# Kernel optimization log

Hardware: AMD Instinct MI355X
Metric: run time of the kernel (lower is better)

Reference implementation:

```python
import jax, jax.numpy as jnp
import numpy as np

NP, NC, E, EL = 50000, 5000, 200000, 100000
DP, DC, HID, OUT, HEADS = 1280, 256, 128, 128, 4


def setup_inputs() -> dict:
    key = jax.random.key(0)
    ks = jax.random.split(key, 40)
    p = lambda k, shp: jax.random.normal(k, shp, dtype=jnp.float32) * 0.05
    inp = {
        "x_protein": jax.random.normal(ks[0], (NP, DP), dtype=jnp.float32),
        "x_class": jax.random.normal(ks[1], (NC, DC), dtype=jnp.float32),
        "src": jax.random.randint(ks[2], (E,), 0, NP),
        "dst": jax.random.randint(ks[3], (E,), 0, NC),
        "edge_label_src": jax.random.randint(ks[4], (EL,), 0, NP),
        "edge_label_dst": jax.random.randint(ks[5], (EL,), 0, NC),
        # SAGEConv, relation protein->class (updates class nodes)
        "sage_pc_Wl": p(ks[6], (DP, HID)), "sage_pc_bl": p(ks[7], (HID,)), "sage_pc_Wr": p(ks[8], (DC, HID)),
        # SAGEConv, relation class->protein (updates protein nodes)
        "sage_cp_Wl": p(ks[9], (DC, HID)), "sage_cp_bl": p(ks[10], (HID,)), "sage_cp_Wr": p(ks[11], (DP, HID)),
        # GATConv p->c (inputs are hidden after conv1)
        "gat_pc_Wsrc": p(ks[12], (HID, HEADS * HID)), "gat_pc_Wdst": p(ks[13], (HID, HEADS * HID)),
        "gat_pc_asrc": p(ks[14], (HEADS, HID)), "gat_pc_adst": p(ks[15], (HEADS, HID)), "gat_pc_b": p(ks[16], (HID,)),
        # GATConv c->p
        "gat_cp_Wsrc": p(ks[17], (HID, HEADS * HID)), "gat_cp_Wdst": p(ks[18], (HID, HEADS * HID)),
        "gat_cp_asrc": p(ks[19], (HEADS, HID)), "gat_cp_adst": p(ks[20], (HEADS, HID)), "gat_cp_b": p(ks[21], (HID,)),
        # final per-node-type Linear (to_hetero duplicates lin per node type)
        "lin_p_W": p(ks[22], (HID, OUT)), "lin_p_b": p(ks[23], (OUT,)),
        "lin_c_W": p(ks[24], (HID, OUT)), "lin_c_b": p(ks[25], (OUT,)),
        # link predictor
        "link_W": p(ks[26], (2 * OUT, 1)), "link_b": p(ks[27], (1,)),
    }
    return inp


def _sage(x_src, x_dst, s, d, Wl, bl, Wr, n_dst):
    # PyG SAGEConv: lin_l(mean_aggr(x_src)) + lin_r(x_dst); lin_l has bias.
    agg = jax.ops.segment_sum(x_src[s], d, num_segments=n_dst)
    cnt = jax.ops.segment_sum(jnp.ones((s.shape[0], 1), x_src.dtype), d, num_segments=n_dst)
    mean = agg / jnp.maximum(cnt, 1.0)
    return mean @ Wl + bl + x_dst @ Wr


def _gat(x_src, x_dst, s, d, Ws, Wd, a_s, a_d, b, n_dst):
    # PyG GATConv bipartite, heads=HEADS, concat=False, add_self_loops=False.
    H, C = a_s.shape
    hs = (x_src @ Ws).reshape(-1, H, C)   # [Ns, H, C]
    hd = (x_dst @ Wd).reshape(-1, H, C)   # [Nd, H, C]
    als = jnp.einsum('nhc,hc->nh', hs, a_s)
    ald = jnp.einsum('nhc,hc->nh', hd, a_d)
    e = jax.nn.leaky_relu(als[s] + ald[d], 0.2)                    # [E, H]
    emax = jax.ops.segment_max(e, d, num_segments=n_dst)          # stable softmax per dst
    ee = jnp.exp(e - emax[d])
    denom = jax.ops.segment_sum(ee, d, num_segments=n_dst)
    alpha = ee / denom[d]                                          # [E, H]
    out = jax.ops.segment_sum(alpha[:, :, None] * hs[s], d, num_segments=n_dst)  # [Nd, H, C]
    return out.mean(axis=1) + b  # concat=False -> mean over heads


def reference(x_protein, x_class, src, dst, edge_label_src, edge_label_dst,
              sage_pc_Wl, sage_pc_bl, sage_pc_Wr,
              sage_cp_Wl, sage_cp_bl, sage_cp_Wr,
              gat_pc_Wsrc, gat_pc_Wdst, gat_pc_asrc, gat_pc_adst, gat_pc_b,
              gat_cp_Wsrc, gat_cp_Wdst, gat_cp_asrc, gat_cp_adst, gat_cp_b,
              lin_p_W, lin_p_b, lin_c_W, lin_c_b, link_W, link_b):
    # Layer 1: hetero SAGE (each node type has exactly one incoming relation)
    h_c = jax.nn.relu(_sage(x_protein, x_class, src, dst, sage_pc_Wl, sage_pc_bl, sage_pc_Wr, NC))
    h_p = jax.nn.relu(_sage(x_class, x_protein, dst, src, sage_cp_Wl, sage_cp_bl, sage_cp_Wr, NP))
    # Layer 2: hetero GAT
    g_c = jax.nn.relu(_gat(h_p, h_c, src, dst, gat_pc_Wsrc, gat_pc_Wdst, gat_pc_asrc, gat_pc_adst, gat_pc_b, NC))
    g_p = jax.nn.relu(_gat(h_c, h_p, dst, src, gat_cp_Wsrc, gat_cp_Wdst, gat_cp_asrc, gat_cp_adst, gat_cp_b, NP))
    # Per-type output projection
    z_p = g_p @ lin_p_W + lin_p_b
    z_c = g_c @ lin_c_W + lin_c_b
    # Link predictor: gather, concat, linear, sigmoid
    ef = jnp.concatenate([z_p[edge_label_src], z_c[edge_label_dst]], axis=-1)  # [EL, 2*OUT]
    return jax.nn.sigmoid(ef @ link_W + link_b).squeeze(-1)
```

## Files before the change

### kernel.cpp

```cpp
#include <hip/hip_runtime.h>
#include <math.h>

#define NPROT 50000
#define NCLS  5000
#define DIMP  1280
#define DIMC  256
#define SCAN_N (NCLS + NPROT)
#define KSTEPS (DIMP/32)

#define P1B  ((NPROT+127)/128)
#define C1BY ((NCLS+63)/64)
#define C1B  (4*C1BY)

typedef float4 f4;
typedef __attribute__((ext_vector_type(8))) short short8;
typedef __attribute__((ext_vector_type(4))) float f32x4;

__device__ __forceinline__ unsigned short f2bf(float f){
    unsigned u = __float_as_uint(f);
    u += 0x7FFFu + ((u >> 16) & 1u);
    return (unsigned short)(u >> 16);
}
__device__ __forceinline__ float bf2f(unsigned short b){
    return __uint_as_float(((unsigned)b) << 16);
}
__device__ __forceinline__ void gload_lds16(const void* g, void* l){
    __builtin_amdgcn_global_load_lds((const __attribute__((address_space(1))) void*)g,
                                     (__attribute__((address_space(3))) void*)l, 16, 0, 0);
}
__device__ __forceinline__ int OFFV(const int* __restrict__ offv, const int* __restrict__ part, int v){
    return offv[v] + part[v>>10];
}

__global__ __launch_bounds__(512) void mega1(const float* __restrict__ Af,
                                             const unsigned short* __restrict__ BtP,
                                             unsigned short* __restrict__ P1,
                                             const float* __restrict__ Ac,
                                             const float* __restrict__ WcatC,
                                             float* __restrict__ C1,
                                             const int* __restrict__ src, const int* __restrict__ dst,
                                             const int* __restrict__ offv, const int* __restrict__ part,
                                             int* __restrict__ cur, int* __restrict__ adj, int E){
    __shared__ __align__(16) unsigned char smem[64*1024];
    const int blk = blockIdx.x;
    const int tid = threadIdx.x;

    if(blk < P1B){
        unsigned char* As = smem;
        unsigned char* Bs = smem + 32*1024;
        const int lane = tid & 63;
        const int w    = tid >> 6;
        const int wm   = w >> 2, wn = w & 3;
        const int row0 = blk * 128;
        const int kg = lane >> 4, fr = lane & 15;

        f32x4 acc[4][4] = {};

        auto STAGE = [&](int buf, int k0){
            unsigned char* Ab = As + buf*16384;
            unsigned char* Bb = Bs + buf*16384;
            #pragma unroll
            for(int i=0;i<2;i++){
                int c  = i*512 + tid;
                int r  = c >> 3, cc = c & 7;
                int scc = cc ^ (r & 7);
                int srow = min(row0 + r, NPROT-1);
                gload_lds16((const void*)(Af + (size_t)srow*DIMP + k0 + scc*4),
                            (void*)(Ab + (i*512 + w*64 + lane)*16));
            }
            #pragma unroll
            for(int i=0;i<2;i++){
                int c  = i*512 + tid;
                int r  = c >> 2, cc = c & 3;
                int scc = cc ^ ((r>>1) & 3);
                gload_lds16((const void*)(BtP + (size_t)r*DIMP + k0 + scc*8),
                            (void*)(Bb + (i*512 + w*64 + lane)*16));
            }
        };

        STAGE(0, 0);
        __syncthreads();

        for(int t=0; t<KSTEPS; ++t){
            const int cb = t & 1;
            if(t+1 < KSTEPS) STAGE(cb^1, (t+1)*32);
            const unsigned char* Ab = As + cb*16384;
            const unsigned char* Bb = Bs + cb*16384;

            short8 aF[4], bF[4];
            #pragma unroll
            for(int m=0;m<4;m++){
                int r = wm*64 + m*16 + fr;
                int b0 = r*128 + kg*32;
                f4 lo = *(const f4*)(Ab + (( b0      ) ^ ((r&7)<<4)));
                f4 hi = *(const f4*)(Ab + (( b0 + 16 ) ^ ((r&7)<<4)));
                union { short8 s; unsigned short u[8]; } uu;
                uu.u[0]=f2bf(lo.x); uu.u[1]=f2bf(lo.y); uu.u[2]=f2bf(lo.z); uu.u[3]=f2bf(lo.w);
                uu.u[4]=f2bf(hi.x); uu.u[5]=f2bf(hi.y); uu.u[6]=f2bf(hi.z); uu.u[7]=f2bf(hi.w);
                aF[m] = uu.s;
            }
            #pragma unroll
            for(int n=0;n<4;n++){
                int r = wn*64 + n*16 + fr;
                int b0 = (r*64 + kg*16) ^ (((r>>1)&3)<<4);
                bF[n] = *(const short8*)(Bb + b0);
            }
            #pragma unroll
            for(int m=0;m<4;m++)
            #pragma unroll
            for(int n=0;n<4;n++)
                acc[m][n] = __builtin_amdgcn_mfma_f32_16x16x32_bf16(aF[m], bF[n], acc[m][n], 0, 0, 0);
            __syncthreads();
        }

        #pragma unroll
        for(int m=0;m<4;m++)
        #pragma unroll
        for(int r=0;r<4;r++){
            int row = row0 + wm*64 + m*16 + kg*4 + r;
            if(row < NPROT){
                #pragma unroll
                for(int n=0;n<4;n++)
                    P1[(size_t)row*256 + wn*64 + n*16 + fr] = f2bf(acc[m][n][r]);
            }
        }
    } else if(blk < P1B + C1B){
        float (*As)[68] = (float(*)[68])smem;
        float (*Bs)[64] = (float(*)[64])(smem + 16*68*4);
        const int bi = blk - P1B;
        const int row0 = (bi >> 2) * 64;
        const int col0 = (bi & 3) * 64;
        const bool act = tid < 256;
        const int ty = tid >> 4;
        const int tx = tid & 15;
        const int m  = tid >> 2;
        const int kq = (tid & 3) << 2;
        const int kb = tid >> 4;
        const int c4 = (tid & 15) << 2;

        float acc[4][4];
        #pragma unroll
        for(int i=0;i<4;i++)
        #pragma unroll
            for(int j=0;j<4;j++) acc[i][j]=0.f;

        const bool arow_ok = act && (row0 + m) < NCLS;
        const float* Abase = Ac + (size_t)(row0 + min(m,255)) * DIMC + kq;
        const float* Bbase = WcatC + col0 + c4 + (size_t)kb * 256;

        for(int k0 = 0; k0 < DIMC; k0 += 16){
            if(act){
                f4 av;
                if(arow_ok) av = *(const f4*)(Abase + k0);
                else        av = make_float4(0.f,0.f,0.f,0.f);
                As[kq+0][m]=av.x; As[kq+1][m]=av.y; As[kq+2][m]=av.z; As[kq+3][m]=av.w;
                *(f4*)&Bs[kb][c4] = *(const f4*)(Bbase + (size_t)k0 * 256);
            }
            __syncthreads();
            if(act){
                #pragma unroll
                for(int kk=0;kk<16;kk++){
                    f4 a = *(const f4*)&As[kk][ty<<2];
                    f4 b = *(const f4*)&Bs[kk][tx<<2];
                    float ar[4]={a.x,a.y,a.z,a.w};
                    float br[4]={b.x,b.y,b.z,b.w};
                    #pragma unroll
                    for(int i=0;i<4;i++)
                    #pragma unroll
                        for(int j=0;j<4;j++) acc[i][j] += ar[i]*br[j];
                }
            }
            __syncthreads();
        }
        if(act){
            #pragma unroll
            for(int i=0;i<4;i++){
                int r = row0 + (ty<<2) + i;
                if(r < NCLS){
                    f4 v = make_float4(acc[i][0],acc[i][1],acc[i][2],acc[i][3]);
                    *(f4*)&C1[(size_t)r*256 + col0 + (tx<<2)] = v;
                }
            }
        }
    } else {
        int e = (blk - P1B - C1B)*512 + tid;
        if(e < E){
            int s = src[e], d = dst[e];
            int pc = atomicAdd(&cur[d],1);        adj[OFFV(offv,part,d)+pc] = s;
            int pp = atomicAdd(&cur[NCLS+s],1);   adj[OFFV(offv,part,NCLS+s)+pp] = d;
        }
    }
}

#define NPB ((NPROT+127)/128)
#define NCB ((NCLS+127)/128)
__global__ __launch_bounds__(256) void gemm_hs(const unsigned short* __restrict__ Ap,
                                               const unsigned short* __restrict__ Ac,
                                               const unsigned short* __restrict__ Btp,
                                               const unsigned short* __restrict__ Btc,
                                               const float* __restrict__ projP,
                                               const float* __restrict__ projC,
                                               unsigned short* __restrict__ Cp,
                                               unsigned short* __restrict__ Cc,
                                               float* __restrict__ attP,
                                               float* __restrict__ attC){
    const bool cls = (int)blockIdx.y >= NPB;
    const unsigned short* A  = cls ? Ac : Ap;
    const unsigned short* Bt = cls ? Btc : Btp;
    unsigned short* C = cls ? Cc : Cp;
    const int M = cls ? NCLS : NPROT;
    const int row0 = (cls ? blockIdx.y - NPB : blockIdx.y) * 128;
    const int col0 = blockIdx.x * 128;

    __shared__ __align__(16) unsigned char As[128*32*2];
    __shared__ __align__(16) unsigned char Bs[128*32*2];
    __shared__ float projS[1024];
    const int tid  = threadIdx.x;
    const int lane = tid & 63;
    const int w    = tid >> 6;
    const int wm   = w >> 1, wn = w & 1;
    const int kg = lane >> 4, fr = lane & 15;

    f32x4 acc[4][4] = {};

    for(int k0 = 0; k0 < 128; k0 += 32){
        #pragma unroll
        for(int i=0;i<2;i++){
            int c  = i*256 + w*64 + lane;
            int r  = c >> 2, cc = c & 3;
            int scc = cc ^ ((r>>1) & 3);
            int srow = min(row0 + r, M-1);
            gload_lds16((const void*)(A + (size_t)srow*128 + k0 + scc*8),
                        (void*)(As + (i*256 + w*64)*16));
        }
        #pragma unroll
        for(int i=0;i<2;i++){
            int c  = i*256 + w*64 + lane;
            int r  = c >> 2, cc = c & 3;
            int scc = cc ^ ((r>>1) & 3);
            gload_lds16((const void*)(Bt + (size_t)(col0 + r)*128 + k0 + scc*8),
                        (void*)(Bs + (i*256 + w*64)*16));
        }
        __syncthreads();

        short8 aF[4], bF[4];
        #pragma unroll
        for(int m=0;m<4;m++){
            int r = wm*64 + m*16 + fr;
            int b0 = (r*64 + kg*16) ^ (((r>>1)&3)<<4);
            aF[m] = *(const short8*)(As + b0);
        }
        #pragma unroll
        for(int n=0;n<4;n++){
            int r = wn*64 + n*16 + fr;
            int b0 = (r*64 + kg*16) ^ (((r>>1)&3)<<4);
            bF[n] = *(const short8*)(Bs + b0);
        }
        #pragma unroll
        for(int m=0;m<4;m++)
        #pragma unroll
        for(int n=0;n<4;n++)
            acc[m][n] = __builtin_amdgcn_mfma_f32_16x16x32_bf16(aF[m], bF[n], acc[m][n], 0, 0, 0);
        __syncthreads();
    }

    #pragma unroll
    for(int m=0;m<4;m++)
    #pragma unroll
    for(int r=0;r<4;r++){
        int row = row0 + wm*64 + m*16 + kg*4 + r;
        if(row < M){
            #pragma unroll
            for(int n=0;n<4;n++)
                C[(size_t)row*512 + col0 + wn*64 + n*16 + fr] = f2bf(acc[m][n][r]);
        }
    }

    if(blockIdx.x == 0){
        const float* proj = cls ? projC : projP;
        float* att = cls ? attC : attP;
        for(int i=tid;i<1024;i+=256) projS[i] = proj[i];
        __syncthreads();
        int ri = tid >> 1, cb = (tid & 1)*4;
        int row = row0 + ri;
        if(row < M){
            const unsigned short* ar = A + (size_t)row*128;
            float s0=0.f,s1=0.f,s2=0.f,s3=0.f;
            #pragma unroll
            for(int kk=0;kk<16;kk++){
                short8 a8 = *(const short8*)(ar + kk*8);
                #pragma unroll
                for(int q=0;q<8;q++){
                    float av = bf2f((unsigned short)a8[q]);
                    const float* pr = &projS[(kk*8+q)*8 + cb];
                    s0 += av*pr[0]; s1 += av*pr[1]; s2 += av*pr[2]; s3 += av*pr[3];
                }
            }
            f4 o = make_float4(s0,s1,s2,s3);
            *(f4*)&att[(size_t)row*8 + cb] = o;
        }
    }
}

__global__ void setup(const float* __restrict__ Wl_pc, const float* __restrict__ Wr_cp,
                      const float* __restrict__ Wl_cp, const float* __restrict__ Wr_pc,
                      const float* __restrict__ pcWs, const float* __restrict__ pcAs,
                      const float* __restrict__ pcWd, const float* __restrict__ pcAd,
                      const float* __restrict__ cpWs, const float* __restrict__ cpAs,
                      const float* __restrict__ cpWd, const float* __restrict__ cpAd,
                      const float* __restrict__ lpW, const float* __restrict__ lpb,
                      const float* __restrict__ lcW, const float* __restrict__ lcb,
                      const float* __restrict__ linkW,
                      const int* __restrict__ src, const int* __restrict__ dst,
                      unsigned short* __restrict__ BtP, float* __restrict__ WcatC,
                      unsigned short* __restrict__ BtSp, unsigned short* __restrict__ BtSc,
                      float* __restrict__ projP, float* __restrict__ projC,
                      float* __restrict__ w_p, float* __restrict__ w_c,
                      float* __restrict__ cpc,
                      int* __restrict__ deg, int E){
    int blk = blockIdx.x, tid = threadIdx.x;
    if(blk < 2048){
        int t = blk*256 + tid;
        if(t < 327680){
            int n = t / 1280, k = t % 1280;
            float v = (n<128) ? Wl_pc[(size_t)k*128+n] : Wr_cp[(size_t)k*128+n-128];
            BtP[t] = f2bf(v);
        } else if(t < 393216){
            int i = t - 327680; int k = i>>8, j = i&255;
            WcatC[i] = (j<128) ? Wl_cp[(size_t)k*128+j] : Wr_pc[(size_t)k*128+j-128];
        } else if(t < 458752){
            int i = t - 393216; int n = i>>7, k = i&127;
            BtSp[i] = f2bf(pcWs[(size_t)k*512+n]);
        } else {
            int i = t - 458752; int n = i>>7, k = i&127;
            BtSc[i] = f2bf(cpWs[(size_t)k*512+n]);
        }
    } else if(blk < 2056){
        int sec = (blk-2048) >> 1;
        int t = ((blk-2048) & 1)*256 + tid;
        const float *W, *a; float* proj; int colbase;
        if(sec==0){ W=pcWs; a=pcAs; proj=projP; colbase=0; }
        else if(sec==1){ W=cpWd; a=cpAd; proj=projP; colbase=4; }
        else if(sec==2){ W=pcWd; a=pcAd; proj=projC; colbase=0; }
        else { W=cpWs; a=cpAs; proj=projC; colbase=4; }
        int k = t >> 2, h = t & 3;
        const float* w = W + (size_t)k*512 + h*128;
        const float* av = a + h*128;
        float s=0.f;
        for(int c=0;c<128;c++) s += w[c]*av[c];
        proj[k*8 + colbase + h] = s;
    } else if(blk == 2056){
        if(tid < 128){
            float s=0.f;
            for(int o=0;o<128;o++) s += lpW[(size_t)tid*128+o]*linkW[o];
            w_p[tid]=s;
        } else {
            int j=tid-128;
            float s=0.f;
            for(int o=0;o<128;o++) s += lcW[(size_t)j*128+o]*linkW[128+o];
            w_c[j]=s;
        }
        if(tid==0){ float s=0.f; for(int o=0;o<128;o++) s+=lpb[o]*linkW[o];      cpc[0]=s; }
        if(tid==1){ float s=0.f; for(int o=0;o<128;o++) s+=lcb[o]*linkW[128+o];  cpc[1]=s; }
    } else {
        int e = (blk-2057)*256 + tid;
        if(e < E){
            atomicAdd(&deg[dst[e]],1);
            atomicAdd(&deg[NCLS + src[e]],1);
        }
    }
}

__global__ __launch_bounds__(1024) void scan1(const int* __restrict__ in, int* __restrict__ out,
                                              int* __restrict__ part, int n){
    __shared__ int buf[1024];
    int tid = threadIdx.x;
    int g = blockIdx.x*1024 + tid;
    int v = (g<n) ? in[g] : 0;
    buf[tid] = v;
    __syncthreads();
    for(int o=1;o<1024;o<<=1){
        int t = (tid>=o) ? buf[tid-o] : 0;
        __syncthreads();
        buf[tid] += t;
        __syncthreads();
    }
    if(g<n) out[g] = buf[tid] - v;
    if(tid==1023) part[blockIdx.x] = buf[1023];
}
__global__ __launch_bounds__(64) void scan2(int* __restrict__ part, int nb,
                                            int* __restrict__ offv, int n){
    int tid = threadIdx.x;
    int orig = (tid<nb) ? part[tid] : 0;
    int v = orig;
    #pragma unroll
    for(int o=1;o<64;o<<=1){
        int t = __shfl_up(v, o);
        if(tid>=o) v += t;
    }
    int total = __shfl(v, nb-1);
    if(tid<nb) part[tid] = v - orig;
    if(tid == (n>>10)) offv[n] = total - (v - orig);
}

__global__ __launch_bounds__(256) void sage_all(const int* __restrict__ offv, const int* __restrict__ part,
                                                const int* __restrict__ adj,
                                                const unsigned short* __restrict__ P1, const float* __restrict__ C1,
                                                const float* __restrict__ bl_pc, const float* __restrict__ bl_cp,
                                                unsigned short* __restrict__ h_c, unsigned short* __restrict__ h_p){
    int v = blockIdx.x*4 + (threadIdx.x>>6);
    int l = threadIdx.x & 63;
    if(v >= SCAN_N) return;
    int b = OFFV(offv,part,v), deg = OFFV(offv,part,v+1)-b;
    float a0=0.f, a1=0.f;
    float inv = 1.f/(float)max(deg,1);
    if(v < NCLS){
        for(int i=0;i<deg;i++){
            int s = adj[b+i];
            ushort2 w = *((const ushort2*)P1 + (size_t)s*128 + l);
            a0 += bf2f(w.x); a1 += bf2f(w.y);
        }
        float2 sv = *((const float2*)C1 + (size_t)v*128 + 64 + l);
        float h0 = fmaxf(a0*inv + bl_pc[2*l]   + sv.x, 0.f);
        float h1 = fmaxf(a1*inv + bl_pc[2*l+1] + sv.y, 0.f);
        ushort2 o; o.x=f2bf(h0); o.y=f2bf(h1);
        *((ushort2*)h_c + (size_t)v*64 + l) = o;
    } else {
        int m = v - NCLS;
        for(int i=0;i<deg;i++){
            int d = adj[b+i];
            float2 w = *((const float2*)C1 + (size_t)d*128 + l);
            a0 += w.x; a1 += w.y;
        }
        ushort2 sv = *((const ushort2*)P1 + (size_t)m*128 + 64 + l);
        float h0 = fmaxf(a0*inv + bl_cp[2*l]   + bf2f(sv.x), 0.f);
        float h1 = fmaxf(a1*inv + bl_cp[2*l+1] + bf2f(sv.y), 0.f);
        ushort2 o; o.x=f2bf(h0); o.y=f2bf(h1);
        *((ushort2*)h_p + (size_t)m*64 + l) = o;
    }
}

__global__ __launch_bounds__(128) void gat_all(const int* __restrict__ offv, const int* __restrict__ part,
                                               const int* __restrict__ adj,
                                               const float* __restrict__ attP, const float* __restrict__ attC,
                                               const unsigned short* __restrict__ hs_p,
                                               const unsigned short* __restrict__ hs_c,
                                               const float* __restrict__ gb_pc, const float* __restrict__ gb_cp,
                                               const float* __restrict__ w_c, const float* __restrict__ w_p,
                                               const float* __restrict__ cpc,
                                               float* __restrict__ u_c, float* __restrict__ u_p){
    __shared__ float ald[4];
    __shared__ int   adjS[32];
    __shared__ float eeS[32*4];
    __shared__ float den8[8];
    __shared__ f4    red4[32];

    int n = blockIdx.x;
    const bool cls = n < NCLS;
    const int node = cls ? n : n - NCLS;
    const float* attS = cls ? attP : attC;
    const float* attD = cls ? attC : attP;
    const int abase = cls ? 0 : 4;
    const unsigned short* hs = cls ? hs_p : hs_c;
    const float* gb = cls ? gb_pc : gb_cp;
    const float* wv = cls ? w_c : w_p;
    float* u = cls ? u_c : u_p;
    const int cidx = cls ? 1 : 0;

    int j = threadIdx.x;
    const int hh = j >> 5;
    const int q  = j & 31;
    int b = OFFV(offv,part,n), deg = OFFV(offv,part,n+1)-b;
    if(j < 4) ald[j] = attD[(size_t)node*8 + abase + j];

    float a0=0.f, a1=0.f, a2=0.f, a3=0.f;
    float denP = 0.f;

    for(int base=0; base<deg; base+=32){
        int cnt = min(32, deg-base);
        if(j < cnt) adjS[j] = adj[b+base+j];
        __syncthreads();
        if(j < cnt*4){
            int i = j>>2, h = j&3;
            int s = adjS[i];
            float e = attS[(size_t)s*8 + abase + h] + ald[h];
            e = e > 0.f ? e : 0.2f*e;
            float ee = __expf(e);
            eeS[j] = ee;
            denP += ee;
        }
        __syncthreads();
        for(int ii=0; ii<cnt; ii++){
            int s = adjS[ii];
            float ee = eeS[ii*4 + hh];
            ushort4 v = *(const ushort4*)(hs + (size_t)s*512 + hh*128 + q*4);
            a0 += ee*bf2f(v.x); a1 += ee*bf2f(v.y);
            a2 += ee*bf2f(v.z); a3 += ee*bf2f(v.w);
        }
        __syncthreads();
    }

    float dp = denP;
    dp += __shfl_xor(dp, 4);
    dp += __shfl_xor(dp, 8);
    dp += __shfl_xor(dp, 16);
    dp += __shfl_xor(dp, 32);
    if((j & 63) < 4) den8[(j>>6)*4 + (j&3)] = dp;
    __syncthreads();

    float den_h = den8[hh] + den8[4+hh];
    float inv = (deg > 0) ? 0.25f/den_h : 0.f;
    a0 *= inv; a1 *= inv; a2 *= inv; a3 *= inv;

    a0 += __shfl_xor(a0, 32); a1 += __shfl_xor(a1, 32);
    a2 += __shfl_xor(a2, 32); a3 += __shfl_xor(a3, 32);
    if(j >= 64 && j < 96) red4[q] = make_float4(a0,a1,a2,a3);
    __syncthreads();
    float val = 0.f;
    if(j < 32){
        f4 r = red4[q];
        float t0 = a0 + r.x, t1 = a1 + r.y, t2 = a2 + r.z, t3 = a3 + r.w;
        const float* gbq = gb + q*4;
        const float* wvq = wv + q*4;
        val = fmaxf(t0 + gbq[0], 0.f)*wvq[0]
            + fmaxf(t1 + gbq[1], 0.f)*wvq[1]
            + fmaxf(t2 + gbq[2], 0.f)*wvq[2]
            + fmaxf(t3 + gbq[3], 0.f)*wvq[3];
    }
    #pragma unroll
    for(int o=16;o;o>>=1) val += __shfl_down(val, o);
    if(j == 0) u[node] = val + cpc[cidx];
}

__global__ void link_out(const int* __restrict__ els, const int* __restrict__ eld,
                         const float* __restrict__ u_p, const float* __restrict__ u_c,
                         const float* __restrict__ linkb, float* __restrict__ out, int EL){
    int i = blockIdx.x*256 + threadIdx.x;
    if(i >= EL) return;
    float x = u_p[els[i]] + u_c[eld[i]] + linkb[0];
    out[i] = 1.f/(1.f + __expf(-x));
}

extern "C" void kernel_launch(void* const* d_in, const int* in_sizes, int n_in,
                              void* d_out, int out_size, void* d_ws, size_t ws_size,
                              hipStream_t stream){
    const float* x_p  = (const float*)d_in[0];
    const float* x_c  = (const float*)d_in[1];
    const int*   src  = (const int*)d_in[2];
    const int*   dst  = (const int*)d_in[3];
    const int*   els  = (const int*)d_in[4];
    const int*   eld  = (const int*)d_in[5];
    const float* sage_pc_Wl = (const float*)d_in[6];
    const float* sage_pc_bl = (const float*)d_in[7];
    const float* sage_pc_Wr = (const float*)d_in[8];
    const float* sage_cp_Wl = (const float*)d_in[9];
    const float* sage_cp_bl = (const float*)d_in[10];
    const float* sage_cp_Wr = (const float*)d_in[11];
    const float* gat_pc_Wsrc = (const float*)d_in[12];
    const float* gat_pc_Wdst = (const float*)d_in[13];
    const float* gat_pc_asrc = (const float*)d_in[14];
    const float* gat_pc_adst = (const float*)d_in[15];
    const float* gat_pc_b    = (const float*)d_in[16];
    const float* gat_cp_Wsrc = (const float*)d_in[17];
    const float* gat_cp_Wdst = (const float*)d_in[18];
    const float* gat_cp_asrc = (const float*)d_in[19];
    const float* gat_cp_adst = (const float*)d_in[20];
    const float* gat_cp_b    = (const float*)d_in[21];
    const float* lin_p_W = (const float*)d_in[22];
    const float* lin_p_b = (const float*)d_in[23];
    const float* lin_c_W = (const float*)d_in[24];
    const float* lin_c_b = (const float*)d_in[25];
    const float* link_W  = (const float*)d_in[26];
    const float* link_b  = (const float*)d_in[27];

    const int E  = in_sizes[2];
    const int EL = in_sizes[4];

    float* ws = (float*)d_ws;
    size_t off = 0;
    auto alloc = [&](size_t n)->float*{ float* p = ws + off; off += (n + 3) & ~(size_t)3; return p; };

    unsigned short* BtP  = (unsigned short*)alloc((size_t)256*DIMP/2);
    float* WcatC = alloc((size_t)DIMC*256);
    unsigned short* BtSp = (unsigned short*)alloc((size_t)512*128/2);
    unsigned short* BtSc = (unsigned short*)alloc((size_t)512*128/2);
    unsigned short* P1   = (unsigned short*)alloc((size_t)NPROT*256/2);
    float* C1    = alloc((size_t)NCLS*256);
    unsigned short* h_p  = (unsigned short*)alloc((size_t)NPROT*128/2);
    unsigned short* h_c  = (unsigned short*)alloc((size_t)NCLS*128/2);
    unsigned short* hs_p = (unsigned short*)alloc((size_t)NPROT*512/2);
    unsigned short* hs_c = (unsigned short*)alloc((size_t)NCLS*512/2);
    float* attP  = alloc((size_t)NPROT*8);
    float* attC  = alloc((size_t)NCLS*8);
    float* projP = alloc(128*8);
    float* projC = alloc(128*8);
    float* w_p   = alloc(128);
    float* w_c   = alloc(128);
    float* cpc   = alloc(4);
    int* degcur = (int*)alloc((size_t)2*SCAN_N);
    int* deg = degcur;
    int* cur = degcur + SCAN_N;
    int* offv = (int*)alloc(SCAN_N+1);
    int* part = (int*)alloc(64);
    int* adj  = (int*)alloc((size_t)2*E);
    float* u_p = alloc(NPROT);
    float* u_c = alloc(NCLS);
    if(off*4 > ws_size) return;

    hipMemsetAsync(degcur, 0, (size_t)2*SCAN_N*4, stream);

    setup<<<2057 + (E+255)/256, 256, 0, stream>>>(
        sage_pc_Wl, sage_cp_Wr, sage_cp_Wl, sage_pc_Wr,
        gat_pc_Wsrc, gat_pc_asrc, gat_pc_Wdst, gat_pc_adst,
        gat_cp_Wsrc, gat_cp_asrc, gat_cp_Wdst, gat_cp_adst,
        lin_p_W, lin_p_b, lin_c_W, lin_c_b, link_W,
        src, dst,
        BtP, WcatC, BtSp, BtSc, projP, projC, w_p, w_c, cpc, deg, E);

    const int NB = (SCAN_N + 1023)/1024;
    scan1<<<NB,1024,0,stream>>>(deg, offv, part, SCAN_N);
    scan2<<<1,64,0,stream>>>(part, NB, offv, SCAN_N);

    const int FILLB = (E+511)/512;
    mega1<<<P1B + C1B + FILLB, 512, 0, stream>>>(x_p, BtP, P1, x_c, WcatC, C1,
                                                 src, dst, offv, part, cur, adj, E);

    sage_all<<<(SCAN_N+3)/4,256,0,stream>>>(offv, part, adj, P1, C1, sage_pc_bl, sage_cp_bl, h_c, h_p);

    gemm_hs<<<dim3(4,NPB+NCB),256,0,stream>>>(h_p, h_c, BtSp, BtSc, projP, projC,
                                              hs_p, hs_c, attP, attC);

    gat_all<<<SCAN_N,128,0,stream>>>(offv, part, adj, attP, attC, hs_p, hs_c,
                                     gat_pc_b, gat_cp_b, w_c, w_p, cpc, u_c, u_p);

    link_out<<<(EL+255)/256,256,0,stream>>>(els, eld, u_p, u_c, link_b, (float*)d_out, EL);
}
```

Before: 318.0 us.

## Convert A tile to bf16 at staging time and store C1 as bf16

The protein GEMM now loads fp32 A rows into registers, converts them once to bf16, and writes a bf16 swizzled tile into LDS, replacing the fp32 direct-to-LDS staging and per-fragment conversion. This halves the A tile in LDS (shared memory drops from 64KB to 48KB) and removes repeated conversion work in the MFMA loop, at the cost of register staging and losing the async global-to-LDS path for A. Separately, the class-side projection C1 is stored in bf16, halving the bytes gathered in the SAGE aggregation, with some added precision loss.

```diff
diff --git a/kernel.cpp b/kernel.cpp
--- a/kernel.cpp
+++ b/kernel.cpp
@@ -37,79 +37,81 @@
                                              unsigned short* __restrict__ P1,
                                              const float* __restrict__ Ac,
                                              const float* __restrict__ WcatC,
-                                             float* __restrict__ C1,
+                                             unsigned short* __restrict__ C1,
                                              const int* __restrict__ src, const int* __restrict__ dst,
                                              const int* __restrict__ offv, const int* __restrict__ part,
                                              int* __restrict__ cur, int* __restrict__ adj, int E){
-    __shared__ __align__(16) unsigned char smem[64*1024];
+    __shared__ __align__(16) unsigned char smem[48*1024];
     const int blk = blockIdx.x;
     const int tid = threadIdx.x;
 
     if(blk < P1B){
         unsigned char* As = smem;
-        unsigned char* Bs = smem + 32*1024;
+        unsigned char* Bs = smem + 16*1024;
         const int lane = tid & 63;
         const int w    = tid >> 6;
         const int wm   = w >> 2, wn = w & 3;
         const int row0 = blk * 128;
         const int kg = lane >> 4, fr = lane & 15;
 
+        const int ar_  = tid >> 2;
+        const int acc_ = tid & 3;
+        const int asrow = min(row0 + ar_, NPROT-1);
+        const float* aG = Af + (size_t)asrow*DIMP + acc_*8;
+        const int awoff = ar_*64 + ((acc_ ^ ((ar_>>1)&3)) << 4);
+
         f32x4 acc[4][4] = {};
-
-        auto STAGE = [&](int buf, int k0){
-            unsigned char* Ab = As + buf*16384;
-            unsigned char* Bb = Bs + buf*16384;
-            #pragma unroll
-            for(int i=0;i<2;i++){
-                int c  = i*512 + tid;
-                int r  = c >> 3, cc = c & 7;
-                int scc = cc ^ (r & 7);
-                int srow = min(row0 + r, NPROT-1);
-                gload_lds16((const void*)(Af + (size_t)srow*DIMP + k0 + scc*4),
-                            (void*)(Ab + (i*512 + w*64 + lane)*16));
-            }
+        f4 va, vb;
+
+        auto STAGEB = [&](int buf, int k0){
             #pragma unroll
             for(int i=0;i<2;i++){
                 int c  = i*512 + tid;
                 int r  = c >> 2, cc = c & 3;
                 int scc = cc ^ ((r>>1) & 3);
                 gload_lds16((const void*)(BtP + (size_t)r*DIMP + k0 + scc*8),
-                            (void*)(Bb + (i*512 + w*64 + lane)*16));
+                            (void*)(Bs + buf*16384 + (i*512 + w*64 + lane)*16));
             }
         };
-
-        STAGE(0, 0);
+        auto WRITEA = [&](int buf){
+            union { short8 s; unsigned short u[8]; } uu;
+            uu.u[0]=f2bf(va.x); uu.u[1]=f2bf(va.y); uu.u[2]=f2bf(va.z); uu.u[3]=f2bf(va.w);
+            uu.u[4]=f2bf(vb.x); uu.u[5]=f2bf(vb.y); uu.u[6]=f2bf(vb.z); uu.u[7]=f2bf(vb.w);
+            *(short8*)(As + buf*8192 + awoff) = uu.s;
+        };
+
+        va = *(const f4*)(aG + 0);
+        vb = *(const f4*)(aG + 4);
+        STAGEB(0, 0);
+        WRITEA(0);
         __syncthreads();
 
         for(int t=0; t<KSTEPS; ++t){
             const int cb = t & 1;
-            if(t+1 < KSTEPS) STAGE(cb^1, (t+1)*32);
-            const unsigned char* Ab = As + cb*16384;
-            const unsigned char* Bb = Bs + cb*16384;
+            if(t+1 < KSTEPS){
+                va = *(const f4*)(aG + (t+1)*32);
+                vb = *(const f4*)(aG + (t+1)*32 + 4);
+                STAGEB(cb^1, (t+1)*32);
+            }
 
             short8 aF[4], bF[4];
             #pragma unroll
             for(int m=0;m<4;m++){
                 int r = wm*64 + m*16 + fr;
-                int b0 = r*128 + kg*32;
-                f4 lo = *(const f4*)(Ab + (( b0      ) ^ ((r&7)<<4)));
-                f4 hi = *(const f4*)(Ab + (( b0 + 16 ) ^ ((r&7)<<4)));
-                union { short8 s; unsigned short u[8]; } uu;
-                uu.u[0]=f2bf(lo.x); uu.u[1]=f2bf(lo.y); uu.u[2]=f2bf(lo.z); uu.u[3]=f2bf(lo.w);
-                uu.u[4]=f2bf(hi.x); uu.u[5]=f2bf(hi.y); uu.u[6]=f2bf(hi.z); uu.u[7]=f2bf(hi.w);
-                aF[m] = uu.s;
+                aF[m] = *(const short8*)(As + cb*8192 + r*64 + ((kg ^ ((r>>1)&3))<<4));
             }
             #pragma unroll
             for(int n=0;n<4;n++){
                 int r = wn*64 + n*16 + fr;
-                int b0 = (r*64 + kg*16) ^ (((r>>1)&3)<<4);
-                bF[n] = *(const short8*)(Bb + b0);
+                bF[n] = *(const short8*)(Bs + cb*16384 + r*64 + ((kg ^ ((r>>1)&3))<<4));
             }
             #pragma unroll
             for(int m=0;m<4;m++)
             #pragma unroll
             for(int n=0;n<4;n++)
                 acc[m][n] = __builtin_amdgcn_mfma_f32_16x16x32_bf16(aF[m], bF[n], acc[m][n], 0, 0, 0);
+
+            if(t+1 < KSTEPS) WRITEA(cb^1);
             __syncthreads();
         }
 
@@ -177,8 +179,10 @@
             for(int i=0;i<4;i++){
                 int r = row0 + (ty<<2) + i;
                 if(r < NCLS){
-                    f4 v = make_float4(acc[i][0],acc[i][1],acc[i][2],acc[i][3]);
-                    *(f4*)&C1[(size_t)r*256 + col0 + (tx<<2)] = v;
+                    ushort4 v;
+                    v.x=f2bf(acc[i][0]); v.y=f2bf(acc[i][1]);
+                    v.z=f2bf(acc[i][2]); v.w=f2bf(acc[i][3]);
+                    *(ushort4*)&C1[(size_t)r*256 + col0 + (tx<<2)] = v;
                 }
             }
         }
@@ -405,7 +409,8 @@
 
 __global__ __launch_bounds__(256) void sage_all(const int* __restrict__ offv, const int* __restrict__ part,
                                                 const int* __restrict__ adj,
-                                                const unsigned short* __restrict__ P1, const float* __restrict__ C1,
+                                                const unsigned short* __restrict__ P1,
+                                                const unsigned short* __restrict__ C1,
                                                 const float* __restrict__ bl_pc, const float* __restrict__ bl_cp,
                                                 unsigned short* __restrict__ h_c, unsigned short* __restrict__ h_p){
     int v = blockIdx.x*4 + (threadIdx.x>>6);
@@ -420,17 +425,17 @@
             ushort2 w = *((const ushort2*)P1 + (size_t)s*128 + l);
             a0 += bf2f(w.x); a1 += bf2f(w.y);
         }
-        float2 sv = *((const float2*)C1 + (size_t)v*128 + 64 + l);
-        float h0 = fmaxf(a0*inv + bl_pc[2*l]   + sv.x, 0.f);
-        float h1 = fmaxf(a1*inv + bl_pc[2*l+1] + sv.y, 0.f);
+        ushort2 sv = *((const ushort2*)C1 + (size_t)v*128 + 64 + l);
+        float h0 = fmaxf(a0*inv + bl_pc[2*l]   + bf2f(sv.x), 0.f);
+        float h1 = fmaxf(a1*inv + bl_pc[2*l+1] + bf2f(sv.y), 0.f);
         ushort2 o; o.x=f2bf(h0); o.y=f2bf(h1);
         *((ushort2*)h_c + (size_t)v*64 + l) = o;
     } else {
         int m = v - NCLS;
         for(int i=0;i<deg;i++){
             int d = adj[b+i];
-            float2 w = *((const float2*)C1 + (size_t)d*128 + l);
-            a0 += w.x; a1 += w.y;
+            ushort2 w = *((const ushort2*)C1 + (size_t)d*128 + l);
+            a0 += bf2f(w.x); a1 += bf2f(w.y);
         }
         ushort2 sv = *((const ushort2*)P1 + (size_t)m*128 + 64 + l);
         float h0 = fmaxf(a0*inv + bl_cp[2*l]   + bf2f(sv.x), 0.f);
@@ -585,7 +590,7 @@
     unsigned short* BtSp = (unsigned short*)alloc((size_t)512*128/2);
     unsigned short* BtSc = (unsigned short*)alloc((size_t)512*128/2);
     unsigned short* P1   = (unsigned short*)alloc((size_t)NPROT*256/2);
-    float* C1    = alloc((size_t)NCLS*256);
+    unsigned short* C1   = (unsigned short*)alloc((size_t)NCLS*256/2);
     unsigned short* h_p  = (unsigned short*)alloc((size_t)NPROT*128/2);
     unsigned short* h_c  = (unsigned short*)alloc((size_t)NCLS*128/2);
     unsigned short* hs_p = (unsigned short*)alloc((size_t)NPROT*512/2);
```

Result: faster. 298.6 us (-6.1%).
